# Optimization experiments

Hardware: AMD Instinct MI355X
Metric: run time of the kernel (lower is better)

## Reference

```python
import jax, jax.numpy as jnp
import numpy as np
import math

D = 768; H = 8; HD = D // H; T = 1024; V = 32000; M = 10
BLOCK = 128          # flex-attention block size (sliding_window_num_blocks granularity)
TAU = 1.0            # gumbel_temp
MAXC = 10            # max middle-block visits == scan length
EPS = 1e-6
IFP = 0.95           # initial_forward_prob

def rms(x):
    return x * jax.lax.rsqrt(jnp.mean(x * x, axis=-1, keepdims=True) + EPS)

def make_rope(t):
    # Rotary.__init__: dim//4 real inv freqs + dim//4 zeros -> cos/sin of shape [t, HD//2]
    inv = (1.0 / 1024) ** jnp.linspace(0.0, 1.0, HD // 4)
    inv = jnp.concatenate([inv, jnp.zeros(HD // 4)])
    th = jnp.arange(t, dtype=jnp.float32)[:, None] * inv[None, :]
    return jnp.cos(th), jnp.sin(th)

def rope(x, cos, sin):
    # x: [1,T,H,HD]
    c = cos[None, :, None, :]; s = sin[None, :, None, :]
    x1, x2 = jnp.split(x, 2, axis=-1)
    return jnp.concatenate([x1 * c + x2 * s, -x1 * s + x2 * c], axis=-1)

def attn(x, ve, wq, wk, wv, wo, lam, cos, sin, mask):
    q = (x @ wq.T).reshape(1, T, H, HD)
    k = (x @ wk.T).reshape(1, T, H, HD)
    v = (x @ wv.T).reshape(1, T, H, HD)
    if ve is not None:
        v = lam[0] * v + lam[1] * ve.reshape(1, T, H, HD)
    else:
        v = lam[0] * v
    q = rope(rms(q), cos, sin); k = rope(rms(k), cos, sin)
    sc = jnp.einsum('bthd,bshd->bhts', q, k) * (1.0 / math.sqrt(HD))
    sc = jnp.where(mask, sc, -1e30)
    y = jnp.einsum('bhts,bshd->bthd', jax.nn.softmax(sc, axis=-1), v).reshape(1, T, D)
    return y @ wo.T

def mlp(x, fc, pr):
    return jnp.square(jax.nn.relu(x @ fc.T)) @ pr.T

def fwd(tokens, embed_w, ve_w, lm_head_w,
        in_wq, in_wk, in_wv, in_wo, in_attn_lam, in_fc, in_pr, in_lam,
        mid_wq, mid_wk, mid_wv, mid_wo, mid_attn_lam, mid_fc, mid_pr, router_w, router_b,
        out_wq, out_wk, out_wv, out_wo, out_attn_lam, out_fc, out_pr, out_lam,
        gumbel_u, window_blocks, max_block_count):
    cos, sin = make_rope(T)
    qi = jnp.arange(T)
    mask = ((qi[:, None] >= qi[None, :]) &
            ((qi[:, None] // BLOCK - qi[None, :] // BLOCK) < window_blocks))[None, None]
    x = rms(embed_w[tokens][None])     # norm(embed(inputs))
    x0 = x
    ve = ve_w[tokens][None]            # X=1 value embedding, reused for output block
    # ---- input FixedBlock ----
    h = in_lam[0] * x + in_lam[1] * x0
    h = h + attn(rms(h), ve, in_wq, in_wk, in_wv, in_wo, in_attn_lam, cos, sin, mask)
    h = h + mlp(rms(h), in_fc, in_pr)
    # ---- middle routing loop (fixed-length scan, masked once exited) ----
    g = -jnp.log(-jnp.log(gumbel_u + 1e-10) + 1e-10)  # [MAXC, M+1] gumbel noise
    mbc = jnp.float32(max_block_count)
    def step(carry, gi):
        x, cur, done, cnt = carry
        y = x + attn(rms(x), None, mid_wq[cur], mid_wk[cur], mid_wv[cur], mid_wo[cur],
                     mid_attn_lam[cur], cos, sin, mask)
        y = y + mlp(rms(y), mid_fc[cur], mid_pr[cur])
        feat = jnp.concatenate([y.mean(axis=1), jnp.stack([cnt, mbc])[None]], axis=-1)  # [1, D+2]
        logits = feat @ router_w[cur].T + router_b[cur]                                  # [1, M+1]
        route = jax.nn.softmax((logits + gi[None]) / TAU, axis=-1)
        nxt = jnp.argmax(route[0]).astype(jnp.int32)
        new_cnt = cnt + 1.0
        exit_now = (nxt == M) | (new_cnt >= mbc)
        x = jnp.where(done, x, y)
        cnt = jnp.where(done, cnt, new_cnt)
        new_done = done | exit_now
        cur = jnp.where(new_done, cur, nxt)
        return (x, cur, new_done, cnt), None
    init = (h, jnp.int32(0), jnp.bool_(False), jnp.float32(0.0))
    (x, _, _, _), _ = jax.lax.scan(step, init, g)
    # ---- output FixedBlock ----
    y = out_lam[0] * x + out_lam[1] * x0
    y = y + attn(rms(y), ve, out_wq, out_wk, out_wv, out_wo, out_attn_lam, cos, sin, mask)
    y = y + mlp(rms(y), out_fc, out_pr)
    logits = rms(y) @ lm_head_w.T
    return 30.0 * jnp.tanh(logits / 30.0)

def setup_inputs() -> dict:
    key = jax.random.key(0)
    ks = iter(jax.random.split(key, 64))
    def w(*s, std=0.02):
        return (std * jax.random.normal(next(ks), s)).astype(jnp.float32)
    rb = np.full((M, M + 1), math.log((1.0 - IFP) / M), dtype=np.float32)
    for i in range(M):
        rb[i, min(i + 1, M)] = math.log(IFP)
    inp = {
        'tokens': jax.random.randint(next(ks), (T,), 0, V, dtype=jnp.int32),
        'embed_w': w(V, D), 've_w': w(V, D), 'lm_head_w': w(V, D),
        'in_wq': w(D, D), 'in_wk': w(D, D), 'in_wv': w(D, D), 'in_wo': w(D, D),
        'in_attn_lam': jnp.array([0.5, 0.5], jnp.float32),
        'in_fc': w(4 * D, D), 'in_pr': w(D, 4 * D),
        'in_lam': jnp.array([1.0, 0.0], jnp.float32),
        'mid_wq': w(M, D, D), 'mid_wk': w(M, D, D), 'mid_wv': w(M, D, D), 'mid_wo': w(M, D, D),
        'mid_attn_lam': jnp.tile(jnp.array([0.5, 0.5], jnp.float32), (M, 1)),
        'mid_fc': w(M, 4 * D, D), 'mid_pr': w(M, D, 4 * D),
        'router_w': w(M, M + 1, D + 2, std=0.001),
        'router_b': jnp.asarray(rb),
        'out_wq': w(D, D), 'out_wk': w(D, D), 'out_wv': w(D, D), 'out_wo': w(D, D),
        'out_attn_lam': jnp.array([0.5, 0.5], jnp.float32),
        'out_fc': w(4 * D, D), 'out_pr': w(D, 4 * D),
        'out_lam': jnp.array([1.0, 0.0], jnp.float32),
        'gumbel_u': jax.random.uniform(next(ks), (MAXC, M + 1), dtype=jnp.float32),
        'window_blocks': 4,
        'max_block_count': MAXC,
    }
    return inp

def reference(tokens, embed_w, ve_w, lm_head_w,
              in_wq, in_wk, in_wv, in_wo, in_attn_lam, in_fc, in_pr, in_lam,
              mid_wq, mid_wk, mid_wv, mid_wo, mid_attn_lam, mid_fc, mid_pr, router_w, router_b,
              out_wq, out_wk, out_wv, out_wo, out_attn_lam, out_fc, out_pr, out_lam,
              gumbel_u, window_blocks, max_block_count):
    return fwd(tokens, embed_w, ve_w, lm_head_w,
               in_wq, in_wk, in_wv, in_wo, in_attn_lam, in_fc, in_pr, in_lam,
               mid_wq, mid_wk, mid_wv, mid_wo, mid_attn_lam, mid_fc, mid_pr, router_w, router_b,
               out_wq, out_wk, out_wv, out_wo, out_attn_lam, out_fc, out_pr, out_lam,
               gumbel_u, window_blocks, max_block_count)
```

## Files before the change

### kernel.cpp

```cpp
#include <hip/hip_runtime.h>
#include <hip/hip_bf16.h>

namespace {

constexpr int cT   = 1024;
constexpr int cD   = 768;
constexpr int cH   = 8;
constexpr int cHD  = 96;
constexpr int cM   = 10;
constexpr int cDff = 3072;
constexpr int cV   = 32000;
constexpr int cTD  = cT * cD;
constexpr float cEps = 1e-6f;

constexpr long oWQ = 0;
constexpr long oWK = 589824;
constexpr long oWV = 2L * 589824;
constexpr long oWO = 3L * 589824;
constexpr long oFC = 4L * 589824;
constexpr long oPR = 4L * 589824 + 2359296;
constexpr long cWTOT = 4L * 589824 + 2L * 2359296;
constexpr int cConvBlocks = (int)(cWTOT / 8 / 256);

typedef __attribute__((ext_vector_type(8))) short short8;
typedef __attribute__((ext_vector_type(4))) float f32x4;

__device__ inline short bf16r(float f) {
  union { float f; unsigned u; } x{f};
  unsigned r = (x.u + 0x7FFF + ((x.u >> 16) & 1)) >> 16;
  return (short)r;
}

__device__ inline float bf2f(short s) {
  union { unsigned u; float f; } x;
  x.u = ((unsigned)(unsigned short)s) << 16;
  return x.f;
}


__global__ void init_state_k(int* cur, int* done, float* cnt, float* feat) {
  if (threadIdx.x == 0) { *cur = 0; *done = 0; *cnt = 0.0f; }
  for (int d = threadIdx.x; d < cD; d += 256) feat[d] = 0.f;
}

__global__ void rope_pre_k(float* __restrict__ cosb, float* __restrict__ sinb) {
  int idx = blockIdx.x * blockDim.x + threadIdx.x;
  if (idx >= cT * 48) return;
  int t = idx / 48, j = idx % 48;
  float th = 0.0f;
  if (j < 24) th = (float)t * powf(1.0f / 1024.0f, (float)j / 23.0f);
  cosb[idx] = cosf(th);
  sinb[idx] = sinf(th);
}

__global__ __launch_bounds__(256) void embed_rms_k(const int* __restrict__ tok,
    const float* __restrict__ ew, const float* __restrict__ vw,
    float* __restrict__ x0, float* __restrict__ ve) {
  int t = blockIdx.x;
  int tk = tok[t];
  const float* er = ew + (size_t)tk * cD;
  const float* vr = vw + (size_t)tk * cD;
  __shared__ float red[256];
  float s = 0.f;
  for (int d = threadIdx.x; d < cD; d += 256) { float e = er[d]; s += e * e; }
  red[threadIdx.x] = s; __syncthreads();
  for (int st = 128; st; st >>= 1) { if (threadIdx.x < st) red[threadIdx.x] += red[threadIdx.x + st]; __syncthreads(); }
  float sc = rsqrtf(red[0] / cD + cEps);
  for (int d = threadIdx.x; d < cD; d += 256) {
    x0[(size_t)t * cD + d] = er[d] * sc;
    ve[(size_t)t * cD + d] = vr[d];
  }
}

__global__ __launch_bounds__(256) void rms_rows_bf(const float* __restrict__ in,
    short* __restrict__ out, const int* done) {
  if (done && *done) return;
  int t = blockIdx.x;
  const float* r = in + (size_t)t * cD;
  __shared__ float red[256];
  float s = 0.f;
  for (int d = threadIdx.x; d < cD; d += 256) { float v = r[d]; s += v * v; }
  red[threadIdx.x] = s; __syncthreads();
  for (int st = 128; st; st >>= 1) { if (threadIdx.x < st) red[threadIdx.x] += red[threadIdx.x + st]; __syncthreads(); }
  float sc = rsqrtf(red[0] / cD + cEps);
  short* o = out + (size_t)t * cD;
  for (int d = threadIdx.x; d < cD; d += 256) o[d] = bf16r(r[d] * sc);
}

__global__ void axpy_lam_k(const float* __restrict__ lam, const float* __restrict__ a,
                           const float* __restrict__ b, float* __restrict__ o, int n) {
  int i = blockIdx.x * 256 + threadIdx.x;
  if (i < n) o[i] = lam[0] * a[i] + lam[1] * b[i];
}


__global__ __launch_bounds__(256) void layer_pre_k(const float* __restrict__ s0,
    const float* __restrict__ s1, const float* __restrict__ s2, const float* __restrict__ s3,
    const float* __restrict__ s4, const float* __restrict__ s5, short* __restrict__ dst,
    const int* __restrict__ cur, const int* __restrict__ done,
    const float* __restrict__ xin, short* __restrict__ xnbf, float* __restrict__ rsum) {
  if (done && *done) return;
  const int b = blockIdx.x;
  if (b < cConvBlocks) {
    long e = ((long)b * 256 + threadIdx.x) * 8;
    long cu = cur ? (long)(*cur) : 0L;
    const float* src;
    if (e < oWK)      src = s0 + cu * 589824  + e;
    else if (e < oWV) src = s1 + cu * 589824  + (e - oWK);
    else if (e < oWO) src = s2 + cu * 589824  + (e - oWV);
    else if (e < oFC) src = s3 + cu * 589824  + (e - oWO);
    else if (e < oPR) src = s4 + cu * 2359296 + (e - oFC);
    else              src = s5 + cu * 2359296 + (e - oPR);
    float4 a0 = *(const float4*)src;
    float4 a1 = *(const float4*)(src + 4);
    short8 sv;
    sv[0]=bf16r(a0.x); sv[1]=bf16r(a0.y); sv[2]=bf16r(a0.z); sv[3]=bf16r(a0.w);
    sv[4]=bf16r(a1.x); sv[5]=bf16r(a1.y); sv[6]=bf16r(a1.z); sv[7]=bf16r(a1.w);
    *(short8*)(dst + e) = sv;
  } else {
    const int t = b - cConvBlocks;
    const float* r = xin + (size_t)t * cD;
    __shared__ float red[256];
    float s = 0.f;
    for (int d = threadIdx.x; d < cD; d += 256) { float v = r[d]; s += v * v; }
    red[threadIdx.x] = s; __syncthreads();
    for (int st = 128; st; st >>= 1) { if (threadIdx.x < st) red[threadIdx.x] += red[threadIdx.x + st]; __syncthreads(); }
    float sc = rsqrtf(red[0] / cD + cEps);
    short* o = xnbf + (size_t)t * cD;
    for (int d = threadIdx.x; d < cD; d += 256) o[d] = bf16r(r[d] * sc);
    if (threadIdx.x == 0) rsum[t] = 0.f;
  }
}

__global__ __launch_bounds__(256) void conv1_k(const float* __restrict__ src,
    short* __restrict__ dst, long nchunk) {
  long i = (long)blockIdx.x * 256 + threadIdx.x;
  if (i >= nchunk) return;
  long e = i * 8;
  float4 a0 = *(const float4*)(src + e);
  float4 a1 = *(const float4*)(src + e + 4);
  short8 sv;
  sv[0]=bf16r(a0.x); sv[1]=bf16r(a0.y); sv[2]=bf16r(a0.z); sv[3]=bf16r(a0.w);
  sv[4]=bf16r(a1.x); sv[5]=bf16r(a1.y); sv[6]=bf16r(a1.z); sv[7]=bf16r(a1.w);
  *(short8*)(dst + e) = sv;
}


__global__ __launch_bounds__(256) void qkv_k(const short* __restrict__ A,
    const short* __restrict__ Wb,
    short* __restrict__ qo, short* __restrict__ ko, short* __restrict__ vo,
    const int* __restrict__ done, const float* __restrict__ lamb,
    const int* __restrict__ cur, const float* __restrict__ vep,
    const float* __restrict__ cosb, const float* __restrict__ sinb) {
  if (done && *done) return;
  const int z = blockIdx.z;
  const short* W = Wb + (long)z * 589824L;
  const int h  = blockIdx.x;
  const int bm = blockIdx.y * 64;
  __shared__ short As[2][64][40];
  __shared__ short Bs[2][96][40];
  const int tid = threadIdx.x;
  const int w = tid >> 6, lane = tid & 63;
  const int fr = lane & 15, fg = lane >> 4;
  const int ar = tid >> 2, ac2 = (tid & 3) << 3;
  const int br1 = (256 + tid) >> 2, bc1 = ((256 + tid) & 3) << 3;

  short8 aN, bN0, bN1;
  aN  = *(const short8*)(A + (size_t)(bm + ar) * cD + ac2);
  bN0 = *(const short8*)(W + (size_t)(h * cHD + ar) * cD + ac2);
  if (tid < 128) bN1 = *(const short8*)(W + (size_t)(h * cHD + br1) * cD + bc1);
  *(short8*)&As[0][ar][ac2] = aN;
  *(short8*)&Bs[0][ar][ac2] = bN0;
  if (tid < 128) *(short8*)&Bs[0][br1][bc1] = bN1;
  __syncthreads();

  f32x4 acc[6] = {};
  int cb = 0;
  for (int kt = 0; kt < cD; kt += 32) {
    const int ktn = kt + 32;
    const bool hn = ktn < cD;
    if (hn) {
      aN  = *(const short8*)(A + (size_t)(bm + ar) * cD + ktn + ac2);
      bN0 = *(const short8*)(W + (size_t)(h * cHD + ar) * cD + ktn + ac2);
      if (tid < 128) bN1 = *(const short8*)(W + (size_t)(h * cHD + br1) * cD + ktn + bc1);
    }
    short8 af = *(const short8*)&As[cb][w * 16 + fr][fg * 8];
#pragma unroll
    for (int n = 0; n < 6; ++n) {
      short8 bf = *(const short8*)&Bs[cb][n * 16 + fr][fg * 8];
      acc[n] = __builtin_amdgcn_mfma_f32_16x16x32_bf16(af, bf, acc[n], 0, 0, 0);
    }
    if (hn) {
      *(short8*)&As[cb ^ 1][ar][ac2] = aN;
      *(short8*)&Bs[cb ^ 1][ar][ac2] = bN0;
      if (tid < 128) *(short8*)&Bs[cb ^ 1][br1][bc1] = bN1;
    }
    __syncthreads();
    cb ^= 1;
  }

  const int t0 = bm + w * 16 + fg * 4;
  if (z < 2) {
    float scl[4];
#pragma unroll
    for (int r = 0; r < 4; ++r) {
      float s = 0.f;
#pragma unroll
      for (int n = 0; n < 6; ++n) s += acc[n][r] * acc[n][r];
#pragma unroll
      for (int mm = 1; mm < 16; mm <<= 1) s += __shfl_xor(s, mm, 64);
      scl[r] = rsqrtf(s * (1.0f / 96.0f) + cEps);
    }
    short* C = (z == 0 ? qo : ko);
#pragma unroll
    for (int r = 0; r < 4; ++r) {
      int t = t0 + r;
      short* orow = C + (size_t)t * cD + h * cHD;
#pragma unroll
      for (int n = 0; n < 3; ++n) {
        int j = n * 16 + fr;
        float c = cosb[t * 48 + j], sn = sinb[t * 48 + j];
        float x1 = acc[n][r] * scl[r], x2 = acc[n + 3][r] * scl[r];
        orow[j]      = bf16r(x1 * c + x2 * sn);
        orow[j + 48] = bf16r(-x1 * sn + x2 * c);
      }
    }
  } else {
    int cu = cur ? *cur : 0;
    float l0 = lamb[2 * cu], l1 = lamb[2 * cu + 1];
#pragma unroll
    for (int r = 0; r < 4; ++r) {
      int t = t0 + r;
#pragma unroll
      for (int n = 0; n < 6; ++n) {
        float val = l0 * acc[n][r];
        if (vep) val += l1 * vep[(size_t)t * cD + h * cHD + n * 16 + fr];
        vo[(size_t)t * cD + h * cHD + n * 16 + fr] = bf16r(val);
      }
    }
  }
}


__global__ __launch_bounds__(256) void attn_f(const short* __restrict__ q,
    const short* __restrict__ k, const short* __restrict__ v, short* __restrict__ o,
    const int* __restrict__ wbp, const int* done) {
  if (done && *done) return;
  const int qb = blockIdx.x;
  const int h  = blockIdx.y;
  const int q0 = qb * 64;
  const int qb128 = q0 >> 7;
  const int wb = *wbp;
  int kb_lo = qb128 - wb + 1; if (kb_lo < 0) kb_lo = 0;

  __shared__ short Ksh[128][136];
  __shared__ short Vt[96][136];

  const int tid  = threadIdx.x;
  const int w    = tid >> 6;
  const int lane = tid & 63;
  const int fr   = lane & 15;
  const int fg   = lane >> 4;

  short8 qf[3];
  {
    const short* qrow = q + (size_t)(q0 + w * 16 + fr) * cD + h * cHD;
#pragma unroll
    for (int ks = 0; ks < 3; ++ks) qf[ks] = *(const short8*)(qrow + ks * 32 + fg * 8);
  }

  const int srow = (tid * 6) / 12 + 0;
  (void)srow;

  short8 rK[6], rV[6];
  auto issue = [&](int kb) {
    const int key0 = kb * 128;
#pragma unroll
    for (int c = 0; c < 6; ++c) {
      int idx = c * 256 + tid;
      int row = idx / 12, colc = (idx % 12) * 8;
      rK[c] = *(const short8*)(k + (size_t)(key0 + row) * cD + h * cHD + colc);
      rV[c] = *(const short8*)(v + (size_t)(key0 + row) * cD + h * cHD + colc);
    }
  };

  f32x4 accO[6] = {};
  float mrun[4], lrun[4];
#pragma unroll
  for (int r = 0; r < 4; ++r) { mrun[r] = -1e30f; lrun[r] = 0.f; }

  issue(kb_lo);
  for (int kb = kb_lo; kb <= qb128; ++kb) {
    __syncthreads();
#pragma unroll
    for (int c = 0; c < 6; ++c) {
      int idx = c * 256 + tid;
      int row = idx / 12, colc = (idx % 12) * 8;
      *(short8*)&Ksh[row][colc] = rK[c];
      short8 vv = rV[c];
#pragma unroll
      for (int i = 0; i < 8; ++i) Vt[colc + i][row] = vv[i];
    }
    __syncthreads();
    if (kb < qb128) issue(kb + 1);

    const int key0 = kb * 128;
    f32x4 s[8];
#pragma unroll
    for (int n = 0; n < 8; ++n) s[n] = (f32x4){0.f, 0.f, 0.f, 0.f};
#pragma unroll
    for (int ks = 0; ks < 3; ++ks) {
#pragma unroll
      for (int n = 0; n < 8; ++n) {
        short8 kf = *(const short8*)&Ksh[n * 16 + fr][ks * 32 + fg * 8];
        s[n] = __builtin_amdgcn_mfma_f32_16x16x32_bf16(qf[ks], kf, s[n], 0, 0, 0);
      }
    }

    float pmax[4] = {-1e30f, -1e30f, -1e30f, -1e30f};
#pragma unroll
    for (int n = 0; n < 8; ++n)
#pragma unroll
      for (int r = 0; r < 4; ++r) {
        float val = s[n][r] * 0.10206207261596577f;
        int key  = key0 + n * 16 + fr;
        int qrow = q0 + w * 16 + fg * 4 + r;
        if (key > qrow) val = -1e30f;
        s[n][r] = val;
        pmax[r] = fmaxf(pmax[r], val);
      }
#pragma unroll
    for (int mm = 1; mm < 16; mm <<= 1)
#pragma unroll
      for (int r = 0; r < 4; ++r) pmax[r] = fmaxf(pmax[r], __shfl_xor(pmax[r], mm, 64));
    float alpha[4], psum[4];
#pragma unroll
    for (int r = 0; r < 4; ++r) {
      float mn = fmaxf(mrun[r], pmax[r]);
      alpha[r] = __expf(mrun[r] - mn);
      mrun[r] = mn;
      psum[r] = 0.f;
    }
#pragma unroll
    for (int n = 0; n < 8; ++n)
#pragma unroll
      for (int r = 0; r < 4; ++r) {
        float p = __expf(s[n][r] - mrun[r]);
        s[n][r] = p;
        psum[r] += p;
      }
#pragma unroll
    for (int mm = 1; mm < 16; mm <<= 1)
#pragma unroll
      for (int r = 0; r < 4; ++r) psum[r] += __shfl_xor(psum[r], mm, 64);
#pragma unroll
    for (int r = 0; r < 4; ++r) lrun[r] = lrun[r] * alpha[r] + psum[r];
#pragma unroll
    for (int n = 0; n < 6; ++n) {
      f32x4 t = accO[n];
#pragma unroll
      for (int r = 0; r < 4; ++r) t[r] *= alpha[r];
      accO[n] = t;
    }

    __syncthreads();
#pragma unroll
    for (int n = 0; n < 8; ++n)
#pragma unroll
      for (int r = 0; r < 4; ++r)
        Ksh[w * 16 + fg * 4 + r][n * 16 + fr] = bf16r(s[n][r]);
    __syncthreads();

#pragma unroll
    for (int ks = 0; ks < 4; ++ks) {
      short8 pf = *(const short8*)&Ksh[w * 16 + fr][ks * 32 + fg * 8];
#pragma unroll
      for (int n = 0; n < 6; ++n) {
        short8 vf = *(const short8*)&Vt[n * 16 + fr][ks * 32 + fg * 8];
        accO[n] = __builtin_amdgcn_mfma_f32_16x16x32_bf16(pf, vf, accO[n], 0, 0, 0);
      }
    }
  }

#pragma unroll
  for (int r = 0; r < 4; ++r) {
    float inv = 1.0f / lrun[r];
    int t = q0 + w * 16 + fg * 4 + r;
#pragma unroll
    for (int n = 0; n < 6; ++n)
      o[(size_t)t * cD + h * cHD + n * 16 + fr] = bf16r(accO[n][r] * inv);
  }
}


template <int EPI, typename OT>
__global__ __launch_bounds__(256) void gemm64_k(const short* __restrict__ A,
    const short* __restrict__ W, OT* __restrict__ C, const int* __restrict__ done,
    const float* __restrict__ res, float* __restrict__ rsum, int ld, int kn, int N) {
  if (done && *done) return;
  const int bm = blockIdx.y * 64;
  const int bn = blockIdx.x * 64;
  const int k0 = blockIdx.z * kn;
  __shared__ short As[2][64][40];
  __shared__ short Bs[2][64][40];
  const int tid = threadIdx.x;
  const int wid = tid >> 6, lane = tid & 63;
  const int wr = wid >> 1, wc = wid & 1;
  const int fr = lane & 15, fg = lane >> 4;
  const int ar = tid >> 2, ac = (tid & 3) << 3;

  short8 aN = *(const short8*)(A + (size_t)(bm + ar) * ld + k0 + ac);
  short8 bN = *(const short8*)(W + (size_t)(bn + ar) * ld + k0 + ac);
  *(short8*)&As[0][ar][ac] = aN;
  *(short8*)&Bs[0][ar][ac] = bN;
  __syncthreads();

  f32x4 acc[2][2] = {};
  int cb = 0;
  for (int kt = 0; kt < kn; kt += 32) {
    const int ktn = kt + 32;
    const bool hn = ktn < kn;
    if (hn) {
      aN = *(const short8*)(A + (size_t)(bm + ar) * ld + k0 + ktn + ac);
      bN = *(const short8*)(W + (size_t)(bn + ar) * ld + k0 + ktn + ac);
    }
    short8 af[2], bfv[2];
#pragma unroll
    for (int m = 0; m < 2; ++m) af[m] = *(const short8*)&As[cb][wr * 32 + m * 16 + fr][fg * 8];
#pragma unroll
    for (int n = 0; n < 2; ++n) bfv[n] = *(const short8*)&Bs[cb][wc * 32 + n * 16 + fr][fg * 8];
#pragma unroll
    for (int m = 0; m < 2; ++m)
#pragma unroll
      for (int n = 0; n < 2; ++n)
        acc[m][n] = __builtin_amdgcn_mfma_f32_16x16x32_bf16(af[m], bfv[n], acc[m][n], 0, 0, 0);
    if (hn) {
      *(short8*)&As[cb ^ 1][ar][ac] = aN;
      *(short8*)&Bs[cb ^ 1][ar][ac] = bN;
    }
    __syncthreads();
    cb ^= 1;
  }
#pragma unroll
  for (int m = 0; m < 2; ++m)
#pragma unroll
    for (int r = 0; r < 4; ++r) {
      const int row = bm + wr * 32 + m * 16 + fg * 4 + r;
      float p = 0.f;
#pragma unroll
      for (int n = 0; n < 2; ++n) {
        const int col = bn + wc * 32 + n * 16 + fr;
        float val = acc[m][n][r];
        if constexpr (EPI == 1) {
          val += res[(size_t)row * N + col];
          C[(size_t)row * N + col] = val;
          p += val * val;
        } else {
          C[(size_t)blockIdx.z * cTD + (size_t)row * N + col] = (OT)bf16r(val);
        }
      }
      if constexpr (EPI == 1) {
#pragma unroll
        for (int mm = 1; mm < 16; mm <<= 1) p += __shfl_xor(p, mm, 64);
        if (fr == 0) atomicAdd(&rsum[row], p);
      }
    }
}


__global__ __launch_bounds__(256) void mgemm_fc_k(const float* __restrict__ Ay,
    const float* __restrict__ rsum, const short* __restrict__ W, short* __restrict__ C,
    const int* __restrict__ done, int K, int N) {
  if (done && *done) return;
  const int bm = blockIdx.y * 64;
  const int bn = blockIdx.x * 128;
  __shared__ short As[2][64][40];
  __shared__ short Bs[2][128][40];
  const int tid = threadIdx.x;
  const int wid = tid >> 6, lane = tid & 63;
  const int wr = wid >> 1, wc = wid & 1;
  const int fr = lane & 15, fg = lane >> 4;
  const int ar = tid >> 2, ac = (tid & 3) << 3;
  const int br1 = (256 + tid) >> 2, bc1 = ((256 + tid) & 3) << 3;

  const float ascl = rsqrtf(rsum[bm + ar] * (1.0f / cD) + cEps);
  const float* arow = Ay + (size_t)(bm + ar) * K;

  auto loadA = [&](int kt) -> short8 {
    float4 a0 = *(const float4*)(arow + kt + ac);
    float4 a1 = *(const float4*)(arow + kt + ac + 4);
    short8 sv;
    sv[0]=bf16r(a0.x*ascl); sv[1]=bf16r(a0.y*ascl); sv[2]=bf16r(a0.z*ascl); sv[3]=bf16r(a0.w*ascl);
    sv[4]=bf16r(a1.x*ascl); sv[5]=bf16r(a1.y*ascl); sv[6]=bf16r(a1.z*ascl); sv[7]=bf16r(a1.w*ascl);
    return sv;
  };

  short8 aN, bN0, bN1;
  aN  = loadA(0);
  bN0 = *(const short8*)(W + (size_t)(bn + ar) * K + ac);
  bN1 = *(const short8*)(W + (size_t)(bn + br1) * K + bc1);
  *(short8*)&As[0][ar][ac] = aN;
  *(short8*)&Bs[0][ar][ac] = bN0;
  *(short8*)&Bs[0][br1][bc1] = bN1;
  __syncthreads();

  f32x4 acc[2][4] = {};
  int cb = 0;
  for (int kt = 0; kt < K; kt += 32) {
    const int ktn = kt + 32;
    const bool hn = ktn < K;
    if (hn) {
      aN  = loadA(ktn);
      bN0 = *(const short8*)(W + (size_t)(bn + ar) * K + ktn + ac);
      bN1 = *(const short8*)(W + (size_t)(bn + br1) * K + ktn + bc1);
    }
    short8 af[2], bfv[4];
#pragma unroll
    for (int m = 0; m < 2; ++m) af[m] = *(const short8*)&As[cb][wr * 32 + m * 16 + fr][fg * 8];
#pragma unroll
    for (int n = 0; n < 4; ++n) bfv[n] = *(const short8*)&Bs[cb][wc * 64 + n * 16 + fr][fg * 8];
#pragma unroll
    for (int m = 0; m < 2; ++m)
#pragma unroll
      for (int n = 0; n < 4; ++n)
        acc[m][n] = __builtin_amdgcn_mfma_f32_16x16x32_bf16(af[m], bfv[n], acc[m][n], 0, 0, 0);
    if (hn) {
      *(short8*)&As[cb ^ 1][ar][ac] = aN;
      *(short8*)&Bs[cb ^ 1][ar][ac] = bN0;
      *(short8*)&Bs[cb ^ 1][br1][bc1] = bN1;
    }
    __syncthreads();
    cb ^= 1;
  }
#pragma unroll
  for (int m = 0; m < 2; ++m)
#pragma unroll
    for (int n = 0; n < 4; ++n)
#pragma unroll
      for (int r = 0; r < 4; ++r) {
        int row = bm + wr * 32 + m * 16 + fg * 4 + r;
        int col = bn + wc * 64 + n * 16 + fr;
        float val = acc[m][n][r];
        val = fmaxf(val, 0.f); val = val * val;
        C[(size_t)row * N + col] = bf16r(val);
      }
}


__global__ __launch_bounds__(256) void reduce_k(const short* __restrict__ pb,
    float* __restrict__ y, float* __restrict__ x, float* __restrict__ feat,
    const int* done) {
  if (done && *done) return;
  __shared__ float red[256];
  const int d = blockIdx.x * 32 + (threadIdx.x & 31);
  const int tc = threadIdx.x >> 5;
  const int t0 = blockIdx.y * 128 + tc * 16;
  float s = 0.f;
  for (int t = t0; t < t0 + 16; ++t) {
    size_t i = (size_t)t * cD + d;
    float v = y[i];
#pragma unroll
    for (int z = 0; z < 4; ++z) v += bf2f(pb[(size_t)z * cTD + i]);
    y[i] = v;
    if (x) x[i] = v;
    s += v;
  }
  if (feat) {
    red[threadIdx.x] = s; __syncthreads();
    if (threadIdx.x < 32) {
      float tot = 0.f;
#pragma unroll
      for (int c = 0; c < 8; ++c) tot += red[c * 32 + threadIdx.x];
      atomicAdd(&feat[d], tot * (1.0f / cT));
    }
  }
}


__global__ void router_step_k(float* __restrict__ feat, const float* __restrict__ rw,
    const float* __restrict__ rb, const float* __restrict__ gu, int iter,
    const int* __restrict__ mbcp, int* cur, int* done, float* cnt) {
  if (*done) return;
  __shared__ float lg[cM + 1];
  const int tid = threadIdx.x;
  const int c = *cur;
  const float mbc = (float)(*mbcp);
  const float cn = *cnt;
  for (int j = 0; j < cM + 1; ++j) {
    const float* w = rw + ((size_t)c * (cM + 1) + j) * (cD + 2);
    float s = 0.f;
    for (int d = tid; d < cD; d += 64) s += feat[d] * w[d];
#pragma unroll
    for (int mm = 32; mm; mm >>= 1) s += __shfl_xor(s, mm, 64);
    if (tid == 0) {
      s += cn * w[cD] + mbc * w[cD + 1] + rb[c * (cM + 1) + j];
      float u = gu[iter * (cM + 1) + j];
      float inner = -logf(u + 1e-10f) + 1e-10f;
      lg[j] = s - logf(inner);
    }
  }
  __syncthreads();
  for (int d = tid; d < cD; d += 64) feat[d] = 0.f;
  if (tid == 0) {
    int nxt = 0; float best = lg[0];
    for (int j = 1; j < cM + 1; ++j) if (lg[j] > best) { best = lg[j]; nxt = j; }
    float nc = cn + 1.0f;
    int ex = (nxt == cM) || (nc >= mbc);
    *cnt = nc;
    if (ex) *done = 1; else *cur = nxt;
  }
}


__global__ __launch_bounds__(256) void gemm_lm_k(const short* __restrict__ A,
    const short* __restrict__ W, float* __restrict__ C) {
  const int nwg = (cV / 128) * (cT / 128);
  const int cpx = nwg / 8;
  const int swz = (blockIdx.x % 8) * cpx + blockIdx.x / 8;
  const int bm = (swz & 7) * 128;
  const int bn = (swz >> 3) * 128;
  __shared__ short As[2][128][40];
  __shared__ short Bs[2][128][40];
  const int tid = threadIdx.x;
  const int wid = tid >> 6, lane = tid & 63;
  const int wr = wid >> 1, wc = wid & 1;
  const int fr = lane & 15, fg = lane >> 4;
  const int r0 = tid >> 2, c0 = (tid & 3) << 3;
  const int r1 = (256 + tid) >> 2, c1 = ((256 + tid) & 3) << 3;

  short8 aN0, aN1, bN0, bN1;
  aN0 = *(const short8*)(A + (size_t)(bm + r0) * cD + c0);
  aN1 = *(const short8*)(A + (size_t)(bm + r1) * cD + c1);
  bN0 = *(const short8*)(W + (size_t)(bn + r0) * cD + c0);
  bN1 = *(const short8*)(W + (size_t)(bn + r1) * cD + c1);
  *(short8*)&As[0][r0][c0] = aN0;
  *(short8*)&As[0][r1][c1] = aN1;
  *(short8*)&Bs[0][r0][c0] = bN0;
  *(short8*)&Bs[0][r1][c1] = bN1;
  __syncthreads();

  f32x4 acc[4][4] = {};
  int cb = 0;
  for (int kt = 0; kt < cD; kt += 32) {
    const int ktn = kt + 32;
    const bool hn = ktn < cD;
    if (hn) {
      aN0 = *(const short8*)(A + (size_t)(bm + r0) * cD + ktn + c0);
      aN1 = *(const short8*)(A + (size_t)(bm + r1) * cD + ktn + c1);
      bN0 = *(const short8*)(W + (size_t)(bn + r0) * cD + ktn + c0);
      bN1 = *(const short8*)(W + (size_t)(bn + r1) * cD + ktn + c1);
    }
    short8 af[4], bfv[4];
#pragma unroll
    for (int m = 0; m < 4; ++m) af[m] = *(const short8*)&As[cb][wr * 64 + m * 16 + fr][fg * 8];
#pragma unroll
    for (int n = 0; n < 4; ++n) bfv[n] = *(const short8*)&Bs[cb][wc * 64 + n * 16 + fr][fg * 8];
#pragma unroll
    for (int m = 0; m < 4; ++m)
#pragma unroll
      for (int n = 0; n < 4; ++n)
        acc[m][n] = __builtin_amdgcn_mfma_f32_16x16x32_bf16(af[m], bfv[n], acc[m][n], 0, 0, 0);
    if (hn) {
      *(short8*)&As[cb ^ 1][r0][c0] = aN0;
      *(short8*)&As[cb ^ 1][r1][c1] = aN1;
      *(short8*)&Bs[cb ^ 1][r0][c0] = bN0;
      *(short8*)&Bs[cb ^ 1][r1][c1] = bN1;
    }
    __syncthreads();
    cb ^= 1;
  }
#pragma unroll
  for (int m = 0; m < 4; ++m)
#pragma unroll
    for (int n = 0; n < 4; ++n)
#pragma unroll
      for (int r = 0; r < 4; ++r) {
        int row = bm + wr * 64 + m * 16 + fg * 4 + r;
        int col = bn + wc * 64 + n * 16 + fr;
        C[(size_t)row * cV + col] = 30.f * tanhf(acc[m][n][r] * (1.f / 30.f));
      }
}

}


extern "C" void kernel_launch(void* const* d_in, const int* in_sizes, int n_in,
                              void* d_out, int out_size, void* d_ws, size_t ws_size,
                              hipStream_t stream) {
  const int*   tokens    = (const int*)d_in[0];
  const float* embed_w   = (const float*)d_in[1];
  const float* ve_w      = (const float*)d_in[2];
  const float* lm_head_w = (const float*)d_in[3];
  const float* in_wq  = (const float*)d_in[4];
  const float* in_wk  = (const float*)d_in[5];
  const float* in_wv  = (const float*)d_in[6];
  const float* in_wo  = (const float*)d_in[7];
  const float* in_al  = (const float*)d_in[8];
  const float* in_fc  = (const float*)d_in[9];
  const float* in_pr  = (const float*)d_in[10];
  const float* in_lam = (const float*)d_in[11];
  const float* mid_wq = (const float*)d_in[12];
  const float* mid_wk = (const float*)d_in[13];
  const float* mid_wv = (const float*)d_in[14];
  const float* mid_wo = (const float*)d_in[15];
  const float* mid_al = (const float*)d_in[16];
  const float* mid_fc = (const float*)d_in[17];
  const float* mid_pr = (const float*)d_in[18];
  const float* router_w = (const float*)d_in[19];
  const float* router_b = (const float*)d_in[20];
  const float* out_wq = (const float*)d_in[21];
  const float* out_wk = (const float*)d_in[22];
  const float* out_wv = (const float*)d_in[23];
  const float* out_wo = (const float*)d_in[24];
  const float* out_al = (const float*)d_in[25];
  const float* out_fc = (const float*)d_in[26];
  const float* out_pr = (const float*)d_in[27];
  const float* out_lam = (const float*)d_in[28];
  const float* gumbel_u = (const float*)d_in[29];
  const int*   wbp  = (const int*)d_in[30];
  const int*   mbcp = (const int*)d_in[31];
  float* outp = (float*)d_out;

  float* ws = (float*)d_ws;
  float* xb   = ws;
  float* x0b  = xb  + cTD;
  float* veb  = x0b + cTD;
  float* yb   = veb + cTD;
  float* cosb = yb  + cTD;
  float* sinb = cosb + cT * 48;
  float* rsum = sinb + cT * 48;
  float* feat = rsum + 1024;
  int*   curp  = (int*)(feat + 784);
  int*   donep = curp + 1;
  float* cntp  = (float*)(curp + 2);
  short* xnbf  = (short*)(feat + 784 + 8);
  short* aobf  = xnbf + cTD;
  short* qbf   = aobf + cTD;
  short* kbf   = qbf  + cTD;
  short* vbf   = kbf  + cTD;
  short* pbuf  = aobf;
  short* hidbf = vbf  + cTD;
  short* wbf   = hidbf + (size_t)cT * cDff;

  const dim3 gPre(cConvBlocks + cT, 1, 1);
  const dim3 gQKV(cH, cT / 64, 3);
  const dim3 gWO(cD / 64, cT / 64, 1);
  const dim3 gPR(cD / 64, cT / 64, 4);
  const dim3 gFF(cDff / 128, cT / 64, 1);
  const dim3 gLM(2000, 1, 1);
  const dim3 gAttn(cT / 64, cH, 1);
  const dim3 gRed(cD / 32, 8, 1);
  const long lmChunks = (long)cV * cD / 8;
  const int gConvLM = (int)(lmChunks / 256);

  auto layer = [&](const float* wq, const float* wk, const float* wv, const float* wo,
                   const float* alam, const float* fc, const float* pr,
                   const int* cur, const int* done,
                   float* xin, float* yout, const float* vept,
                   float* xcom, float* featp) {
    layer_pre_k<<<gPre, 256, 0, stream>>>(wq, wk, wv, wo, fc, pr, wbf, cur, done,
                                          xin, xnbf, rsum);
    qkv_k<<<gQKV, 256, 0, stream>>>(xnbf, wbf, qbf, kbf, vbf, done, alam, cur, vept,
                                    cosb, sinb);
    attn_f<<<gAttn, 256, 0, stream>>>(qbf, kbf, vbf, aobf, wbp, done);
    gemm64_k<1, float><<<gWO, 256, 0, stream>>>(aobf, wbf + oWO, yout, done, xin, rsum,
                                                cD, cD, cD);
    mgemm_fc_k<<<gFF, 256, 0, stream>>>(yout, rsum, wbf + oFC, hidbf, done, cD, cDff);
    gemm64_k<4, short><<<gPR, 256, 0, stream>>>(hidbf, wbf + oPR, pbuf, done, nullptr,
                                                nullptr, cDff, cDff / 4, cD);
    reduce_k<<<gRed, 256, 0, stream>>>(pbuf, yout, xcom, featp, done);
  };

  init_state_k<<<1, 256, 0, stream>>>(curp, donep, cntp, feat);
  rope_pre_k<<<(cT * 48 + 255) / 256, 256, 0, stream>>>(cosb, sinb);
  embed_rms_k<<<cT, 256, 0, stream>>>(tokens, embed_w, ve_w, x0b, veb);

  axpy_lam_k<<<cTD / 256, 256, 0, stream>>>(in_lam, x0b, x0b, xb, cTD);
  layer(in_wq, in_wk, in_wv, in_wo, in_al, in_fc, in_pr, nullptr, nullptr,
        xb, xb, veb, nullptr, nullptr);

  for (int it = 0; it < cM; ++it) {
    layer(mid_wq, mid_wk, mid_wv, mid_wo, mid_al, mid_fc, mid_pr,
          curp, donep, xb, yb, nullptr, xb, feat);
    router_step_k<<<1, 64, 0, stream>>>(feat, router_w, router_b, gumbel_u, it, mbcp,
                                        curp, donep, cntp);
  }

  axpy_lam_k<<<cTD / 256, 256, 0, stream>>>(out_lam, xb, x0b, xb, cTD);
  layer(out_wq, out_wk, out_wv, out_wo, out_al, out_fc, out_pr, nullptr, nullptr,
        xb, xb, veb, nullptr, nullptr);

  conv1_k<<<gConvLM, 256, 0, stream>>>(lm_head_w, wbf, lmChunks);
  rms_rows_bf<<<cT, 256, 0, stream>>>(xb, xnbf, nullptr);
  gemm_lm_k<<<gLM, 256, 0, stream>>>(xnbf, wbf, outp);
}
```

Before: 2.146 ms.

## Double-buffer weight conversion and overlap it with reduce and embed kernels

Converting the next layer's fp32 weights to bf16 now happens speculatively inside earlier kernels (embed, reduce) writing into two alternating slots, and the lm_head conversion is folded into the last reduce. Each middle iteration's pre-kernel skips the conversion when the router kept the predicted block index. This hides the memory-bound conversion behind other work and removes standalone conversion kernels. In exchange it needs extra workspace for two weight slots plus a separate lm_head buffer, and does wasted conversion work when the prediction is wrong.

New measurement: 2.158 ms. No clear change (+0.6%).

```diff
diff --git a/kernel.cpp b/kernel.cpp
--- a/kernel.cpp
+++ b/kernel.cpp
@@ -21,6 +21,8 @@
 constexpr long oPR = 4L * 589824 + 2359296;
 constexpr long cWTOT = 4L * 589824 + 2L * 2359296;
 constexpr int cConvBlocks = (int)(cWTOT / 8 / 256);
+constexpr long cLM = (long)cV * cD;
+constexpr int cConvLMBlocks = (int)(cLM / 8 / 256);
 
 typedef __attribute__((ext_vector_type(8))) short short8;
 typedef __attribute__((ext_vector_type(4))) float f32x4;
@@ -35,6 +37,29 @@
   union { unsigned u; float f; } x;
   x.u = ((unsigned)(unsigned short)s) << 16;
   return x.f;
+}
+
+__device__ inline short8 cvt8(const float* __restrict__ p) {
+  float4 a0 = *(const float4*)p;
+  float4 a1 = *(const float4*)(p + 4);
+  short8 sv;
+  sv[0]=bf16r(a0.x); sv[1]=bf16r(a0.y); sv[2]=bf16r(a0.z); sv[3]=bf16r(a0.w);
+  sv[4]=bf16r(a1.x); sv[5]=bf16r(a1.y); sv[6]=bf16r(a1.z); sv[7]=bf16r(a1.w);
+  return sv;
+}
+
+__device__ inline void conv6(const float* s0, const float* s1, const float* s2,
+    const float* s3, const float* s4, const float* s5, long cu,
+    short* __restrict__ dst, long cb) {
+  long e = (cb * 256 + threadIdx.x) * 8;
+  const float* src;
+  if (e < oWK)      src = s0 + cu * 589824L + e;
+  else if (e < oWV) src = s1 + cu * 589824L + (e - oWK);
+  else if (e < oWO) src = s2 + cu * 589824L + (e - oWV);
+  else if (e < oFC) src = s3 + cu * 589824L + (e - oWO);
+  else if (e < oPR) src = s4 + cu * 2359296L + (e - oFC);
+  else              src = s5 + cu * 2359296L + (e - oPR);
+  *(short8*)(dst + e) = cvt8(src);
 }
 
 
@@ -55,8 +80,15 @@
 
 __global__ __launch_bounds__(256) void embed_rms_k(const int* __restrict__ tok,
     const float* __restrict__ ew, const float* __restrict__ vw,
-    float* __restrict__ x0, float* __restrict__ ve) {
-  int t = blockIdx.x;
+    float* __restrict__ x0, float* __restrict__ ve,
+    const float* iq, const float* ik, const float* iv, const float* io,
+    const float* if_, const float* ip, short* __restrict__ cdst) {
+  const int b = blockIdx.x;
+  if (b >= cT) {
+    conv6(iq, ik, iv, io, if_, ip, 0, cdst, b - cT);
+    return;
+  }
+  int t = b;
   int tk = tok[t];
   const float* er = ew + (size_t)tk * cD;
   const float* vr = vw + (size_t)tk * cD;
@@ -87,6 +119,22 @@
   for (int d = threadIdx.x; d < cD; d += 256) o[d] = bf16r(r[d] * sc);
 }
 
+__global__ __launch_bounds__(256) void rms_pre_k(const float* __restrict__ in,
+    short* __restrict__ out, float* __restrict__ rsum, const int* done) {
+  if (done && *done) return;
+  int t = blockIdx.x;
+  const float* r = in + (size_t)t * cD;
+  __shared__ float red[256];
+  float s = 0.f;
+  for (int d = threadIdx.x; d < cD; d += 256) { float v = r[d]; s += v * v; }
+  red[threadIdx.x] = s; __syncthreads();
+  for (int st = 128; st; st >>= 1) { if (threadIdx.x < st) red[threadIdx.x] += red[threadIdx.x + st]; __syncthreads(); }
+  float sc = rsqrtf(red[0] / cD + cEps);
+  short* o = out + (size_t)t * cD;
+  for (int d = threadIdx.x; d < cD; d += 256) o[d] = bf16r(r[d] * sc);
+  if (threadIdx.x == 0) rsum[t] = 0.f;
+}
+
 __global__ void axpy_lam_k(const float* __restrict__ lam, const float* __restrict__ a,
                            const float* __restrict__ b, float* __restrict__ o, int n) {
   int i = blockIdx.x * 256 + threadIdx.x;
@@ -94,29 +142,17 @@
 }
 
 
-__global__ __launch_bounds__(256) void layer_pre_k(const float* __restrict__ s0,
+__global__ __launch_bounds__(256) void fix_pre_k(const float* __restrict__ s0,
     const float* __restrict__ s1, const float* __restrict__ s2, const float* __restrict__ s3,
     const float* __restrict__ s4, const float* __restrict__ s5, short* __restrict__ dst,
-    const int* __restrict__ cur, const int* __restrict__ done,
+    const int* __restrict__ cur, const int* __restrict__ done, int expected,
     const float* __restrict__ xin, short* __restrict__ xnbf, float* __restrict__ rsum) {
   if (done && *done) return;
   const int b = blockIdx.x;
   if (b < cConvBlocks) {
-    long e = ((long)b * 256 + threadIdx.x) * 8;
-    long cu = cur ? (long)(*cur) : 0L;
-    const float* src;
-    if (e < oWK)      src = s0 + cu * 589824  + e;
-    else if (e < oWV) src = s1 + cu * 589824  + (e - oWK);
-    else if (e < oWO) src = s2 + cu * 589824  + (e - oWV);
-    else if (e < oFC) src = s3 + cu * 589824  + (e - oWO);
-    else if (e < oPR) src = s4 + cu * 2359296 + (e - oFC);
-    else              src = s5 + cu * 2359296 + (e - oPR);
-    float4 a0 = *(const float4*)src;
-    float4 a1 = *(const float4*)(src + 4);
-    short8 sv;
-    sv[0]=bf16r(a0.x); sv[1]=bf16r(a0.y); sv[2]=bf16r(a0.z); sv[3]=bf16r(a0.w);
-    sv[4]=bf16r(a1.x); sv[5]=bf16r(a1.y); sv[6]=bf16r(a1.z); sv[7]=bf16r(a1.w);
-    *(short8*)(dst + e) = sv;
+    const int c = cur ? *cur : 0;
+    if (c == expected) return;
+    conv6(s0, s1, s2, s3, s4, s5, c, dst, b);
   } else {
     const int t = b - cConvBlocks;
     const float* r = xin + (size_t)t * cD;
@@ -130,19 +166,6 @@
     for (int d = threadIdx.x; d < cD; d += 256) o[d] = bf16r(r[d] * sc);
     if (threadIdx.x == 0) rsum[t] = 0.f;
   }
-}
-
-__global__ __launch_bounds__(256) void conv1_k(const float* __restrict__ src,
-    short* __restrict__ dst, long nchunk) {
-  long i = (long)blockIdx.x * 256 + threadIdx.x;
-  if (i >= nchunk) return;
-  long e = i * 8;
-  float4 a0 = *(const float4*)(src + e);
-  float4 a1 = *(const float4*)(src + e + 4);
-  short8 sv;
-  sv[0]=bf16r(a0.x); sv[1]=bf16r(a0.y); sv[2]=bf16r(a0.z); sv[3]=bf16r(a0.w);
-  sv[4]=bf16r(a1.x); sv[5]=bf16r(a1.y); sv[6]=bf16r(a1.z); sv[7]=bf16r(a1.w);
-  *(short8*)(dst + e) = sv;
 }
 
 
@@ -269,9 +292,6 @@
     for (int ks = 0; ks < 3; ++ks) qf[ks] = *(const short8*)(qrow + ks * 32 + fg * 8);
   }
 
-  const int srow = (tid * 6) / 12 + 0;
-  (void)srow;
-
   short8 rK[6], rV[6];
   auto issue = [&](int kb) {
     const int key0 = kb * 128;
@@ -549,7 +569,24 @@
 
 __global__ __launch_bounds__(256) void reduce_k(const short* __restrict__ pb,
     float* __restrict__ y, float* __restrict__ x, float* __restrict__ feat,
-    const int* done) {
+    const int* done,
+    const float* cs0, const float* cs1, const float* cs2,
+    const float* cs3, const float* cs4, const float* cs5,
+    const float* csLM, long cexp, short* __restrict__ cdst,
+    int cmode, int ungated) {
+  if (blockIdx.x >= cD / 32) {
+    if (!ungated && done && *done) return;
+    long cb = (long)(blockIdx.x - cD / 32) * gridDim.y + blockIdx.y;
+    if (cmode == 0) {
+      if (cb < cConvBlocks) conv6(cs0, cs1, cs2, cs3, cs4, cs5, cexp, cdst, cb);
+    } else {
+      if (cb < cConvLMBlocks) {
+        long e = (cb * 256 + threadIdx.x) * 8;
+        *(short8*)(cdst + e) = cvt8(csLM + e);
+      }
+    }
+    return;
+  }
   if (done && *done) return;
   __shared__ float red[256];
   const int d = blockIdx.x * 32 + (threadIdx.x & 31);
@@ -740,57 +777,94 @@
   short* vbf   = kbf  + cTD;
   short* pbuf  = aobf;
   short* hidbf = vbf  + cTD;
-  short* wbf   = hidbf + (size_t)cT * cDff;
-
-  const dim3 gPre(cConvBlocks + cT, 1, 1);
+  short* slot0 = hidbf + (size_t)cT * cDff;
+  short* slot1 = slot0 + cWTOT;
+  short* lmw   = slot1 + cWTOT;
+
+  const dim3 gFix(cConvBlocks + cT, 1, 1);
+  const dim3 gEmbed(cT + cConvBlocks, 1, 1);
   const dim3 gQKV(cH, cT / 64, 3);
   const dim3 gWO(cD / 64, cT / 64, 1);
   const dim3 gPR(cD / 64, cT / 64, 4);
   const dim3 gFF(cDff / 128, cT / 64, 1);
   const dim3 gLM(2000, 1, 1);
   const dim3 gAttn(cT / 64, cH, 1);
-  const dim3 gRed(cD / 32, 8, 1);
-  const long lmChunks = (long)cV * cD / 8;
-  const int gConvLM = (int)(lmChunks / 256);
-
-  auto layer = [&](const float* wq, const float* wk, const float* wv, const float* wo,
-                   const float* alam, const float* fc, const float* pr,
-                   const int* cur, const int* done,
-                   float* xin, float* yout, const float* vept,
-                   float* xcom, float* featp) {
-    layer_pre_k<<<gPre, 256, 0, stream>>>(wq, wk, wv, wo, fc, pr, wbf, cur, done,
-                                          xin, xnbf, rsum);
-    qkv_k<<<gQKV, 256, 0, stream>>>(xnbf, wbf, qbf, kbf, vbf, done, alam, cur, vept,
-                                    cosb, sinb);
+  const dim3 gRedC(cD / 32 + 432, 8, 1);
+  const dim3 gRedLM(cD / 32 + 1500, 8, 1);
+
+  auto body = [&](const short* slot, const int* cur, const int* done,
+                  float* xin, float* yout, const float* vept) {
+    qkv_k<<<gQKV, 256, 0, stream>>>(xnbf, slot, qbf, kbf, vbf, done,
+                                    cur ? mid_al : (vept ? (xin == xb && yout == xb && vept ? in_al : in_al) : in_al),
+                                    cur, vept, cosb, sinb);
     attn_f<<<gAttn, 256, 0, stream>>>(qbf, kbf, vbf, aobf, wbp, done);
-    gemm64_k<1, float><<<gWO, 256, 0, stream>>>(aobf, wbf + oWO, yout, done, xin, rsum,
+    gemm64_k<1, float><<<gWO, 256, 0, stream>>>(aobf, slot + oWO, yout, done, xin, rsum,
                                                 cD, cD, cD);
-    mgemm_fc_k<<<gFF, 256, 0, stream>>>(yout, rsum, wbf + oFC, hidbf, done, cD, cDff);
-    gemm64_k<4, short><<<gPR, 256, 0, stream>>>(hidbf, wbf + oPR, pbuf, done, nullptr,
+    mgemm_fc_k<<<gFF, 256, 0, stream>>>(yout, rsum, slot + oFC, hidbf, done, cD, cDff);
+    gemm64_k<4, short><<<gPR, 256, 0, stream>>>(hidbf, slot + oPR, pbuf, done, nullptr,
                                                 nullptr, cDff, cDff / 4, cD);
-    reduce_k<<<gRed, 256, 0, stream>>>(pbuf, yout, xcom, featp, done);
   };
+  (void)body;
 
   init_state_k<<<1, 256, 0, stream>>>(curp, donep, cntp, feat);
   rope_pre_k<<<(cT * 48 + 255) / 256, 256, 0, stream>>>(cosb, sinb);
-  embed_rms_k<<<cT, 256, 0, stream>>>(tokens, embed_w, ve_w, x0b, veb);
+  embed_rms_k<<<gEmbed, 256, 0, stream>>>(tokens, embed_w, ve_w, x0b, veb,
+                                          in_wq, in_wk, in_wv, in_wo, in_fc, in_pr, slot1);
 
   axpy_lam_k<<<cTD / 256, 256, 0, stream>>>(in_lam, x0b, x0b, xb, cTD);
-  layer(in_wq, in_wk, in_wv, in_wo, in_al, in_fc, in_pr, nullptr, nullptr,
-        xb, xb, veb, nullptr, nullptr);
+  rms_pre_k<<<cT, 256, 0, stream>>>(xb, xnbf, rsum, nullptr);
+  qkv_k<<<gQKV, 256, 0, stream>>>(xnbf, slot1, qbf, kbf, vbf, nullptr, in_al,
+                                  nullptr, veb, cosb, sinb);
+  attn_f<<<gAttn, 256, 0, stream>>>(qbf, kbf, vbf, aobf, wbp, nullptr);
+  gemm64_k<1, float><<<gWO, 256, 0, stream>>>(aobf, slot1 + oWO, xb, nullptr, xb, rsum,
+                                              cD, cD, cD);
+  mgemm_fc_k<<<gFF, 256, 0, stream>>>(xb, rsum, slot1 + oFC, hidbf, nullptr, cD, cDff);
+  gemm64_k<4, short><<<gPR, 256, 0, stream>>>(hidbf, slot1 + oPR, pbuf, nullptr, nullptr,
+                                              nullptr, cDff, cDff / 4, cD);
+  reduce_k<<<gRedC, 256, 0, stream>>>(pbuf, xb, nullptr, nullptr, nullptr,
+                                      mid_wq, mid_wk, mid_wv, mid_wo, mid_fc, mid_pr,
+                                      nullptr, 0L, slot0, 0, 1);
 
   for (int it = 0; it < cM; ++it) {
-    layer(mid_wq, mid_wk, mid_wv, mid_wo, mid_al, mid_fc, mid_pr,
-          curp, donep, xb, yb, nullptr, xb, feat);
+    short* slot  = (it & 1) ? slot1 : slot0;
+    short* nslot = (it & 1) ? slot0 : slot1;
+    fix_pre_k<<<gFix, 256, 0, stream>>>(mid_wq, mid_wk, mid_wv, mid_wo, mid_fc, mid_pr,
+                                        slot, curp, donep, it, xb, xnbf, rsum);
+    qkv_k<<<gQKV, 256, 0, stream>>>(xnbf, slot, qbf, kbf, vbf, donep, mid_al,
+                                    curp, nullptr, cosb, sinb);
+    attn_f<<<gAttn, 256, 0, stream>>>(qbf, kbf, vbf, aobf, wbp, donep);
+    gemm64_k<1, float><<<gWO, 256, 0, stream>>>(aobf, slot + oWO, yb, donep, xb, rsum,
+                                                cD, cD, cD);
+    mgemm_fc_k<<<gFF, 256, 0, stream>>>(yb, rsum, slot + oFC, hidbf, donep, cD, cDff);
+    gemm64_k<4, short><<<gPR, 256, 0, stream>>>(hidbf, slot + oPR, pbuf, donep, nullptr,
+                                                nullptr, cDff, cDff / 4, cD);
+    if (it < cM - 1) {
+      reduce_k<<<gRedC, 256, 0, stream>>>(pbuf, yb, xb, feat, donep,
+                                          mid_wq, mid_wk, mid_wv, mid_wo, mid_fc, mid_pr,
+                                          nullptr, (long)(it + 1), nslot, 0, 0);
+    } else {
+      reduce_k<<<gRedC, 256, 0, stream>>>(pbuf, yb, xb, feat, donep,
+                                          out_wq, out_wk, out_wv, out_wo, out_fc, out_pr,
+                                          nullptr, 0L, slot0, 0, 1);
+    }
     router_step_k<<<1, 64, 0, stream>>>(feat, router_w, router_b, gumbel_u, it, mbcp,
                                         curp, donep, cntp);
   }
 
   axpy_lam_k<<<cTD / 256, 256, 0, stream>>>(out_lam, xb, x0b, xb, cTD);
-  layer(out_wq, out_wk, out_wv, out_wo, out_al, out_fc, out_pr, nullptr, nullptr,
-        xb, xb, veb, nullptr, nullptr);
-
-  conv1_k<<<gConvLM, 256, 0, stream>>>(lm_head_w, wbf, lmChunks);
+  rms_pre_k<<<cT, 256, 0, stream>>>(xb, xnbf, rsum, nullptr);
+  qkv_k<<<gQKV, 256, 0, stream>>>(xnbf, slot0, qbf, kbf, vbf, nullptr, out_al,
+                                  nullptr, veb, cosb, sinb);
+  attn_f<<<gAttn, 256, 0, stream>>>(qbf, kbf, vbf, aobf, wbp, nullptr);
+  gemm64_k<1, float><<<gWO, 256, 0, stream>>>(aobf, slot0 + oWO, xb, nullptr, xb, rsum,
+                                              cD, cD, cD);
+  mgemm_fc_k<<<gFF, 256, 0, stream>>>(xb, rsum, slot0 + oFC, hidbf, nullptr, cD, cDff);
+  gemm64_k<4, short><<<gPR, 256, 0, stream>>>(hidbf, slot0 + oPR, pbuf, nullptr, nullptr,
+                                              nullptr, cDff, cDff / 4, cD);
+  reduce_k<<<gRedLM, 256, 0, stream>>>(pbuf, xb, nullptr, nullptr, nullptr,
+                                       nullptr, nullptr, nullptr, nullptr, nullptr, nullptr,
+                                       lm_head_w, 0L, lmw, 1, 1);
+
   rms_rows_bf<<<cT, 256, 0, stream>>>(xb, xnbf, nullptr);
-  gemm_lm_k<<<gLM, 256, 0, stream>>>(xnbf, wbf, outp);
-}
+  gemm_lm_k<<<gLM, 256, 0, stream>>>(xnbf, lmw, outp);
+}
```
